# Kernel tuning notes

Hardware: AMD Instinct MI355X
Metric: run time of the kernel (lower is better)

Reference implementation:

```python
import jax, jax.numpy as jnp
import numpy as np
from jax import lax

D = 30   # embedding_dim (hardcoded in repo)
Q = 30   # question length
N = 4000 # number of sentences in doc
S = 100  # tokens per sentence
K = 5    # k_for_maxpool
SLOPE = 0.1  # LeakyReLU negative slope


def setup_inputs() -> dict:
    key = jax.random.key(0)
    ks = jax.random.split(key, 20)
    rn = lambda k, sh: jax.random.normal(k, sh, dtype=jnp.float32)
    ru = lambda k, sh: jax.random.uniform(k, sh, dtype=jnp.float32)
    return {
        "doc_sents_embeds": rn(ks[0], (N, S, D)),
        "sents_gaf": ru(ks[1], (N, 3)),
        "question_embeds": rn(ks[2], (Q, D)),
        "q_idfs": ru(ks[3], (Q, 1)),
        "doc_gaf": ru(ks[4], (4,)),
        "conv1_w": rn(ks[5], (D, D, 3)) * 0.1,
        "conv1_b": rn(ks[6], (D,)) * 0.1,
        "conv2_w": rn(ks[7], (D, D, 3)) * 0.1,
        "conv2_b": rn(ks[8], (D,)) * 0.1,
        "qw_W": rn(ks[9], (1, D + 1)) * 0.1,
        "qw_b": rn(ks[10], (1,)) * 0.1,
        "lq1_W": rn(ks[11], (8, 6)) * 0.1,
        "lq1_b": rn(ks[12], (8,)) * 0.1,
        "lq2_W": rn(ks[13], (1, 8)) * 0.1,
        "lq2_b": rn(ks[14], (1,)) * 0.1,
        "so_W": rn(ks[15], (1, 4)) * 0.1,
        "so_b": rn(ks[16], (1,)) * 0.1,
        "fl_W": rn(ks[17], (1, 5)) * 0.1,
        "fl_b": rn(ks[18], (1,)) * 0.1,
    }


def _leaky(x):
    return jnp.where(x >= 0, x, SLOPE * x)


def _conv_block(x, w, b):
    # x: [B, L, D]. torch Conv1d(D, D, 3, padding=2) then slice [1:L+1]
    # is exactly a 'same' conv with padding 1 on each side; then residual add.
    y = lax.conv_general_dilated(x.transpose(0, 2, 1), w, (1,), [(1, 1)],
                                 dimension_numbers=("NCH", "OIH", "NCH"))
    y = _leaky(y + b[None, :, None])
    return y.transpose(0, 2, 1) + x


def _cos_sim(A, B):
    # A: [Q, D], B: [N, S, D] -> [N, Q, S] (num/den as in torch my_cosine_sim)
    num = jnp.einsum("qd,nsd->nqs", A, B)
    den = jnp.linalg.norm(A, axis=-1)[None, :, None] * jnp.linalg.norm(B, axis=-1)[:, None, :]
    return num / den


def _pool(sim):
    # sort-based k-max pooling -> [max, avg_of_top_k]; sim: [N, Q, S] -> [N, Q, 2]
    vals = lax.top_k(sim, K)[0]  # descending
    return jnp.stack([vals[..., 0], vals.mean(-1)], axis=-1)


def reference(doc_sents_embeds, sents_gaf, question_embeds, q_idfs, doc_gaf,
              conv1_w, conv1_b, conv2_w, conv2_b, qw_W, qw_b,
              lq1_W, lq1_b, lq2_W, lq2_b, so_W, so_b, fl_W, fl_b):
    # question context (two residual trigram convs)
    q_conv = _conv_block(question_embeds[None], conv1_w, conv1_b)
    q_conv = _conv_block(q_conv, conv2_w, conv2_b)[0]          # [Q, D]
    # question term weights
    qw_in = jnp.concatenate([q_conv, q_idfs], axis=-1)          # [Q, D+1]
    q_weights = jax.nn.softmax((qw_in @ qw_W.T + qw_b)[:, 0])   # [Q]
    # sentence context convs (batched over all sentences)
    conv_res = _conv_block(doc_sents_embeds, conv1_w, conv1_b)
    conv_res = _conv_block(conv_res, conv2_w, conv2_b)          # [N, S, D]
    # similarity matrices
    sim_insens = _cos_sim(question_embeds, doc_sents_embeds)    # [N, Q, S]
    sim_oh = (sim_insens > 1.0 - 1e-3).astype(sim_insens.dtype)
    sim_sens = _cos_sim(q_conv, conv_res)
    # k-max pooling and per-q tiny MLP attention
    feats = jnp.concatenate([_pool(sim_oh), _pool(sim_insens), _pool(sim_sens)], axis=-1)  # [N, Q, 6]
    lo = _leaky(feats @ lq1_W.T + lq1_b) @ lq2_W.T + lq2_b      # [N, Q, 1]
    lo = lo[..., 0] * q_weights[None, :]
    sent_emit = lo.sum(-1) / Q                                  # [N]
    # per-sentence output layer
    sent_feats = jnp.concatenate([sents_gaf, sent_emit[:, None]], axis=-1)  # [N, 4]
    sent_scores = jax.nn.sigmoid((sent_feats @ so_W.T + so_b)[:, 0])        # [N]
    # doc-level score
    doc_rep = jnp.concatenate([jnp.max(sent_scores)[None], doc_gaf])        # [5]
    final = doc_rep @ fl_W.T + fl_b                                          # [1]
    return final, sent_scores
```

## Files before the change

kernel.cpp:

```cpp
#include <hip/hip_runtime.h>
#include <hip/hip_bf16.h>

#define SLOPE 0.1f

#define OFF_QW    1816
#define OFF_QNI   1846
#define OFF_QNS   1876
#define OFF_QNN   1906
#define OFF_B1    4606
#define OFF_B2    7336
#define OFF_LQ1W  7366
#define OFF_LQ1B  7414
#define OFF_LQ2W  7422
#define OFF_LQ2B  7430
#define OFF_SOW   7431
#define OFF_SOB   7435
#define OFF_FLW   7436
#define OFF_FLB   7441
#define U16_QEA   16384
#define U16_QCA   17408
#define U16_WB1   18432
#define U16_WB2   21504

typedef __attribute__((ext_vector_type(8))) __bf16 bf16x8;
typedef __attribute__((ext_vector_type(4))) float f32x4;

union Frag { uint4 u4; uint u[4]; bf16x8 v; };

__device__ __forceinline__ float bf2f(ushort h) {
    union { uint u; float f; } c; c.u = ((uint)h) << 16; return c.f;
}
__device__ __forceinline__ ushort f2bf(float f) {
    union { float f; uint u; } c; c.f = f;
    uint u = c.u;
    return (ushort)((u + 0x7FFFu + ((u >> 16) & 1u)) >> 16);
}
__device__ __forceinline__ float ldx(const void* p, long i, int bf) {
    if (bf) return bf2f(((const ushort*)p)[i]);
    return ((const float*)p)[i];
}
__device__ __forceinline__ uint pk2(float lo, float hi) {
    uint r;
    asm("v_cvt_pk_bf16_f32 %0, %1, %2" : "=v"(r) : "v"(lo), "v"(hi));
    return r;
}
__device__ __forceinline__ float blo(uint u) { return __uint_as_float(u << 16); }
__device__ __forceinline__ float bhi(uint u) { return __uint_as_float(u & 0xFFFF0000u); }
__device__ __forceinline__ float lk(float x) { return fmaxf(x, SLOPE * x); }

#define CE(x, y) { float _hi = fmaxf(x, y), _lo = fminf(x, y); x = _hi; y = _lo; }

__device__ __forceinline__ void sort4d(float& a, float& b, float& c, float& d) {
    CE(a, b); CE(c, d); CE(a, c); CE(b, d); CE(b, c);
}
__device__ __forceinline__ void merge44_5(const float* a, const float* b, float* t) {
    t[0] = fmaxf(a[0], b[0]);
    t[1] = fmaxf(fminf(a[0], b[0]), fmaxf(a[1], b[1]));
    t[2] = fmaxf(fmaxf(fminf(a[0], b[1]), fminf(a[1], b[0])), fmaxf(a[2], b[2]));
    t[3] = fmaxf(fmaxf(fminf(a[0], b[2]), fminf(a[1], b[1])),
                 fmaxf(fminf(a[2], b[0]), fmaxf(a[3], b[3])));
    t[4] = fmaxf(fmaxf(fminf(a[0], b[3]), fminf(a[1], b[2])),
                 fmaxf(fminf(a[2], b[1]), fminf(a[3], b[0])));
}
__device__ __forceinline__ void merge54_5(const float* a, const float* b, float* t) {
    t[0] = fmaxf(a[0], b[0]);
    t[1] = fmaxf(fminf(a[0], b[0]), fmaxf(a[1], b[1]));
    t[2] = fmaxf(fmaxf(fminf(a[0], b[1]), fminf(a[1], b[0])), fmaxf(a[2], b[2]));
    t[3] = fmaxf(fmaxf(fminf(a[0], b[2]), fminf(a[1], b[1])),
                 fmaxf(fminf(a[2], b[0]), fmaxf(a[3], b[3])));
    t[4] = fmaxf(fmaxf(fmaxf(fminf(a[0], b[3]), fminf(a[1], b[2])),
                       fmaxf(fminf(a[2], b[1]), fminf(a[3], b[0]))), a[4]);
}
__device__ __forceinline__ void merge55_5(const float* a, const float* b, float* t) {
    t[0] = fmaxf(a[0], b[0]);
    t[1] = fmaxf(fminf(a[0], b[0]), fmaxf(a[1], b[1]));
    t[2] = fmaxf(fmaxf(fminf(a[0], b[1]), fminf(a[1], b[0])), fmaxf(a[2], b[2]));
    t[3] = fmaxf(fmaxf(fminf(a[0], b[2]), fminf(a[1], b[1])),
                 fmaxf(fminf(a[2], b[0]), fmaxf(a[3], b[3])));
    t[4] = fmaxf(fmaxf(fmaxf(fminf(a[0], b[3]), fminf(a[1], b[2])),
                       fmaxf(fminf(a[2], b[1]), fminf(a[3], b[0]))),
                 fmaxf(a[4], b[4]));
}

__device__ __forceinline__ int detect_bf(const void* doc_in, int tid, int* scnt) {
    if (tid == 0) *scnt = 0;
    __syncthreads();
    const ushort* p = (const ushort*)doc_in;
    int local = 0;
    for (int i = tid; i < 4096; i += 256) {
        unsigned e = (p[i] >> 7) & 0xFFu;
        if (e != 0u && (e < 100u || e > 134u)) local++;
    }
    atomicAdd(scnt, local);
    __syncthreads();
    return (*scnt > 200) ? 0 : 1;
}

__global__ __launch_bounds__(256) void k_prep(
        const void* doc_in,
        const void* qe_in, const void* qidf_in,
        const void* w1_in, const void* b1_in,
        const void* w2_in, const void* b2_in,
        const void* qwW_in, const void* qwb_in,
        const void* lq1W_in, const void* lq1b_in,
        const void* lq2W_in, const void* lq2b_in,
        const void* soW_in, const void* sob_in,
        const void* flW_in, const void* flb_in,
        float* ws) {
    const int tid = threadIdx.x;
    const int blk = blockIdx.x;
    __shared__ float QE[900], T1[900], QC[900], W[2700], IDF[32], LG[32];
    __shared__ int scnt;

    const int bf = detect_bf(doc_in, tid, &scnt);
    ushort* wsu = (ushort*)ws;

    if (blk == 1) {
        if (tid == 0) { ((int*)ws)[0] = bf; }
        if (tid < 30) ws[OFF_B1 + tid] = ldx(b1_in, tid, bf);
        if (tid < 48) ws[OFF_LQ1W + tid] = ldx(lq1W_in, tid, bf);
        if (tid < 8)  { ws[OFF_LQ1B + tid] = ldx(lq1b_in, tid, bf);
                        ws[OFF_LQ2W + tid] = ldx(lq2W_in, tid, bf); }
        if (tid < 4)  ws[OFF_SOW + tid] = ldx(soW_in, tid, bf);
        if (tid < 5)  ws[OFF_FLW + tid] = ldx(flW_in, tid, bf);
        if (tid == 1) { ws[OFF_LQ2B] = ldx(lq2b_in, 0, bf);
                        ws[OFF_SOB]  = ldx(sob_in, 0, bf);
                        ws[OFF_FLB]  = ldx(flb_in, 0, bf); }
        for (int i = tid; i < 3072; i += 256) {
            int o = i / 96, kk = i % 96;
            float v1 = 0.f;
            if (o < 30 && kk < 90) {
                int ii = kk % 30, k = kk / 30;
                v1 = ldx(w1_in, (long)o*90 + ii*3 + k, bf);
            }
            wsu[U16_WB1 + i] = f2bf(v1);
        }
        return;
    }
    if (blk == 2) {
        if (tid < 30) ws[OFF_B2 + tid] = ldx(b2_in, tid, bf);
        for (int i = tid; i < 3072; i += 256) {
            int o = i / 96, kk = i % 96;
            float v2 = 0.f;
            if (o < 30 && kk < 90) {
                int ii = kk % 30, k = kk / 30;
                v2 = ldx(w2_in, (long)o*90 + ii*3 + k, bf);
            }
            wsu[U16_WB2 + i] = f2bf(v2);
        }
        return;
    }

    if (tid == 0) { ((int*)ws)[0] = bf; }

    for (int i = tid; i < 900; i += 256) QE[i] = ldx(qe_in, i, bf);
    if (tid < 30) IDF[tid] = ldx(qidf_in, tid, bf);
    for (int i = tid; i < 2700; i += 256) W[i] = ldx(w1_in, i, bf);
    __syncthreads();

    for (int idx = tid; idx < 900; idx += 256) {
        int s = idx / 30, o = idx % 30;
        float acc = ldx(b1_in, o, bf);
        for (int k = 0; k < 3; ++k) {
            int t = s + k - 1;
            if (t < 0 || t >= 30) continue;
            for (int i = 0; i < 30; ++i) acc += QE[t*30 + i] * W[o*90 + i*3 + k];
        }
        acc = acc >= 0.f ? acc : SLOPE * acc;
        T1[idx] = acc + QE[idx];
    }
    __syncthreads();
    for (int i = tid; i < 2700; i += 256) W[i] = ldx(w2_in, i, bf);
    __syncthreads();
    for (int idx = tid; idx < 900; idx += 256) {
        int s = idx / 30, o = idx % 30;
        float acc = ldx(b2_in, o, bf);
        for (int k = 0; k < 3; ++k) {
            int t = s + k - 1;
            if (t < 0 || t >= 30) continue;
            for (int i = 0; i < 30; ++i) acc += T1[t*30 + i] * W[o*90 + i*3 + k];
        }
        acc = acc >= 0.f ? acc : SLOPE * acc;
        QC[idx] = acc + T1[idx];
    }
    __syncthreads();

    if (tid < 30) {
        float s1 = 0.f, s2 = 0.f;
        for (int d = 0; d < 30; ++d) {
            float a = QE[tid*30 + d]; s1 += a*a;
            float b = QC[tid*30 + d]; s2 += b*b;
        }
        float n1 = sqrtf(s1);
        ws[OFF_QNN + tid] = n1;
        ws[OFF_QNI + tid] = 1.0f / n1;
        ws[OFF_QNS + tid] = 1.0f / sqrtf(s2);
        float z = ldx(qwb_in, 0, bf);
        for (int d = 0; d < 30; ++d) z += QC[tid*30 + d] * ldx(qwW_in, d, bf);
        z += IDF[tid] * ldx(qwW_in, 30, bf);
        LG[tid] = z;
    }
    __syncthreads();
    if (tid == 0) {
        float m = -1e30f;
        for (int q = 0; q < 30; ++q) m = fmaxf(m, LG[q]);
        float sum = 0.f, e[30];
        for (int q = 0; q < 30; ++q) { e[q] = expf(LG[q] - m); sum += e[q]; }
        for (int q = 0; q < 30; ++q) ws[OFF_QW + q] = e[q] / sum;
    }
    for (int i = tid; i < 1024; i += 256) {
        int q = i >> 5, d = i & 31;
        float ve = (q < 30 && d < 30) ? QE[q*30 + d] : 0.f;
        float vc = (q < 30 && d < 30) ? QC[q*30 + d] : 0.f;
        wsu[U16_QEA + i] = f2bf(ve);
        wsu[U16_QCA + i] = f2bf(vc);
    }
}

__global__ __launch_bounds__(128, 4) void k_main(const void* doc_in, const void* gaf_in,
                                                 void* out, float* ws) {
    const int n = blockIdx.x;
    const int tid = threadIdx.x;
    const int bf = ((const int*)ws)[0];
    const int lane = tid & 63;
    const int wid = tid >> 6;
    const int l15 = lane & 15;
    const int quad = lane >> 4;

    __shared__ uint XA32[1546];
    __shared__ uint XB32[1546];
    __shared__ __align__(16) float INVX[112];
    __shared__ float FE[30][6];

    ushort* XAu = (ushort*)XA32;
    const ushort* wsu = (const ushort*)ws;
    const uint4* qeA = (const uint4*)(wsu + U16_QEA);
    const uint4* qcA = (const uint4*)(wsu + U16_QCA);
    const uint4* wb1 = (const uint4*)(wsu + U16_WB1);
    const uint4* wb2 = (const uint4*)(wsu + U16_WB2);

    float ga0 = ldx(gaf_in, (long)n*3 + 0, bf);
    float ga1 = ldx(gaf_in, (long)n*3 + 1, bf);
    float ga2 = ldx(gaf_in, (long)n*3 + 2, bf);

    for (int i = tid; i < 46; i += 128) {
        int j = (i < 15) ? i : (1500 + i);
        XA32[j] = 0u; XB32[j] = 0u;
    }
    if (tid >= 100 && tid < 112) INVX[tid] = 0.f;
    if (bf) {
        const uint* g = (const uint*)((const ushort*)doc_in + (size_t)n * 3000);
        for (int i = tid; i < 1500; i += 128) XA32[15 + i] = g[i];
    } else {
        const float* p = (const float*)doc_in + (size_t)n * 3000;
        for (int i = tid; i < 3000; i += 128) XAu[30 + i] = f2bf(p[i]);
    }
    __syncthreads();

    if (tid < 100) {
        const uint* r = XA32 + (tid + 1) * 15;
        float s = 0.f;
        #pragma unroll
        for (int i = 0; i < 15; ++i) {
            uint u = r[i];
            float lo = __uint_as_float(u << 16);
            float hi = __uint_as_float(u & 0xFFFF0000u);
            s += lo * lo + hi * hi;
        }
        INVX[tid] = 1.f / sqrtf(s);
    }
    __syncthreads();

    auto sim_pool = [&](const uint4* qa, int iqOff, int fbase, bool do_oh) {
        const int q = wid * 16 + l15;
        Frag b;
        b.u4 = qa[q * 4 + quad];
        f32x4 acc[7];
        #pragma unroll
        for (int mt = 0; mt < 7; ++mt) {
            int m = mt * 16 + l15;
            Frag a;
            if (m < 100) {
                int base = (m + 1) * 15 + quad * 4;
                a.u[0] = XA32[base];     a.u[1] = XA32[base + 1];
                a.u[2] = XA32[base + 2]; a.u[3] = XA32[base + 3];
            } else { a.u[0] = a.u[1] = a.u[2] = a.u[3] = 0u; }
            f32x4 z = {0.f, 0.f, 0.f, 0.f};
            acc[mt] = __builtin_amdgcn_mfma_f32_16x16x32_bf16(a.v, b.v, z, 0, 0, 0);
        }
        const float4* INVX4 = (const float4*)INVX;
        float thr = (do_oh && q < 30) ? 0.999f * ws[OFF_QNN + q] : 1e30f;
        float iq  = (q < 30) ? ws[iqOff + q] : 0.f;
        float g[7][4];
        int cnt = 0;
        #pragma unroll
        for (int mt = 0; mt < 7; ++mt) {
            float4 ix = INVX4[mt * 4 + quad];
            float ixa[4] = {ix.x, ix.y, ix.z, ix.w};
            #pragma unroll
            for (int r = 0; r < 4; ++r) {
                float u = acc[mt][r] * ixa[r];
                if (mt == 6 && (quad * 4 + r) >= 4) u = -1e30f;
                g[mt][r] = u;
                if (do_oh) cnt += (u > thr) ? 1 : 0;
            }
        }
        #pragma unroll
        for (int mt = 0; mt < 7; ++mt) sort4d(g[mt][0], g[mt][1], g[mt][2], g[mt][3]);
        float p0[5], p1[5], p2[5], q0[5], q1[5], t[5];
        merge44_5(g[0], g[1], p0);
        merge44_5(g[2], g[3], p1);
        merge44_5(g[4], g[5], p2);
        merge55_5(p0, p1, q0);
        merge54_5(p2, g[6], q1);
        merge55_5(q0, q1, t);
        #pragma unroll
        for (int d = 16; d < 64; d <<= 1) {
            float pp[5];
            pp[0] = __shfl_xor(t[0], d); pp[1] = __shfl_xor(t[1], d);
            pp[2] = __shfl_xor(t[2], d); pp[3] = __shfl_xor(t[3], d);
            pp[4] = __shfl_xor(t[4], d);
            if (do_oh) cnt += __shfl_xor(cnt, d);
            float tn[5];
            merge55_5(t, pp, tn);
            t[0] = tn[0]; t[1] = tn[1]; t[2] = tn[2]; t[3] = tn[3]; t[4] = tn[4];
        }
        if (quad == 0 && q < 30) {
            if (do_oh) {
                FE[q][0] = cnt > 0 ? 1.f : 0.f;
                FE[q][1] = (float)(cnt > 5 ? 5 : cnt) * 0.2f;
            }
            FE[q][fbase]     = t[0] * iq;
            FE[q][fbase + 1] = (t[0] + t[1] + t[2] + t[3] + t[4]) * 0.2f * iq;
        }
    };

    auto conv_phase = [&](const uint* src32, uint* dst32, const uint4* wb, int bOff,
                          int m0, int m1, int m2, int m3, bool donorm) {
        Frag wf0[3], wf1[3];
        #pragma unroll
        for (int k = 0; k < 3; ++k) {
            wf0[k].u4 = wb[l15 * 12 + k * 4 + quad];
            wf1[k].u4 = wb[(16 + l15) * 12 + k * 4 + quad];
        }
        float b40[4], b41[4];
        #pragma unroll
        for (int r = 0; r < 4; ++r) {
            int o0 = quad * 4 + r, o1 = 16 + quad * 4 + r;
            b40[r] = ws[bOff + o0];
            b41[r] = (o1 < 30) ? ws[bOff + o1] : 0.f;
        }
        auto do_mt = [&](int mt) {
            const int s = mt * 16 + l15;
            const bool sv = (s < 100);
            Frag xf[3];
            #pragma unroll
            for (int k = 0; k < 3; ++k) {
                if (sv) {
                    int base = s * 15 + k * 16 + quad * 4;
                    xf[k].u[0] = src32[base];     xf[k].u[1] = src32[base + 1];
                    xf[k].u[2] = src32[base + 2]; xf[k].u[3] = src32[base + 3];
                } else { xf[k].u[0] = xf[k].u[1] = xf[k].u[2] = xf[k].u[3] = 0u; }
            }
            f32x4 a0 = {0.f, 0.f, 0.f, 0.f}, a1 = {0.f, 0.f, 0.f, 0.f};
            #pragma unroll
            for (int k = 0; k < 3; ++k) {
                a0 = __builtin_amdgcn_mfma_f32_16x16x32_bf16(wf0[k].v, xf[k].v, a0, 0, 0, 0);
                a1 = __builtin_amdgcn_mfma_f32_16x16x32_bf16(wf1[k].v, xf[k].v, a1, 0, 0, 0);
            }
            float ss = 0.f;
            if (sv) {
                const int db = (s + 1) * 15 + quad * 2;
                uint u0 = src32[db],     u1 = src32[db + 1];
                uint u2 = src32[db + 8], u3 = src32[db + 9];
                float v0 = lk(a0[0] + b40[0]) + blo(u0);
                float v1 = lk(a0[1] + b40[1]) + bhi(u0);
                float v2 = lk(a0[2] + b40[2]) + blo(u1);
                float v3 = lk(a0[3] + b40[3]) + bhi(u1);
                dst32[db]     = pk2(v0, v1);
                dst32[db + 1] = pk2(v2, v3);
                float w0 = lk(a1[0] + b41[0]) + blo(u2);
                float w1 = lk(a1[1] + b41[1]) + bhi(u2);
                dst32[db + 8] = pk2(w0, w1);
                ss = v0*v0 + v1*v1 + v2*v2 + v3*v3 + w0*w0 + w1*w1;
                if (quad < 3) {
                    float w2 = lk(a1[2] + b41[2]) + blo(u3);
                    float w3 = lk(a1[3] + b41[3]) + bhi(u3);
                    dst32[db + 9] = pk2(w2, w3);
                    ss += w2*w2 + w3*w3;
                }
            }
            if (donorm) {
                ss += __shfl_xor(ss, 16);
                ss += __shfl_xor(ss, 32);
                if (quad == 0 && sv) INVX[s] = 1.f / sqrtf(ss);
            }
        };
        do_mt(m0); do_mt(m1); do_mt(m2);
        if (m3 >= 0) do_mt(m3);
    };

    sim_pool(qeA, OFF_QNI, 2, true);
    if (wid == 0) conv_phase(XA32, XB32, wb1, OFF_B1, 0, 2, 4, -1, false);
    else          conv_phase(XA32, XB32, wb1, OFF_B1, 1, 3, 5,  6, false);
    __syncthreads();

    if (wid == 0) conv_phase(XB32, XA32, wb2, OFF_B2, 0, 2, 4,  6, true);
    else          conv_phase(XB32, XA32, wb2, OFF_B2, 1, 3, 5, -1, true);
    __syncthreads();

    sim_pool(qcA, OFF_QNS, 4, false);
    __syncthreads();

    if (wid == 0) {
        float val = 0.f;
        if (lane < 30) {
            float lo = ws[OFF_LQ2B];
            #pragma unroll
            for (int j = 0; j < 8; ++j) {
                float h = ws[OFF_LQ1B + j];
                #pragma unroll
                for (int f = 0; f < 6; ++f) h += FE[lane][f] * ws[OFF_LQ1W + j*6 + f];
                h = h >= 0.f ? h : SLOPE * h;
                lo += h * ws[OFF_LQ2W + j];
            }
            val = lo * ws[OFF_QW + lane];
        }
        for (int d = 32; d >= 1; d >>= 1) val += __shfl_xor(val, d);
        if (lane == 0) {
            float emit = val * (1.f / 30.f);
            float z = ws[OFF_SOB];
            z += ga0 * ws[OFF_SOW + 0];
            z += ga1 * ws[OFF_SOW + 1];
            z += ga2 * ws[OFF_SOW + 2];
            z += emit * ws[OFF_SOW + 3];
            float sc = 1.f / (1.f + expf(-z));
            if (bf) ((__hip_bfloat16*)out)[1 + n] = __float2bfloat16(sc);
            else    ((float*)out)[1 + n] = sc;
        }
    }
}

__global__ __launch_bounds__(256) void k_final(const void* docgaf_in, void* out, const float* ws) {
    const int tid = threadIdx.x;
    const int bf = ((const int*)ws)[0];
    __shared__ float red[256];
    float m = -1e30f;
    for (int i = tid; i < 4000; i += 256) {
        float v = bf ? __bfloat162float(((const __hip_bfloat16*)out)[1 + i])
                     : ((const float*)out)[1 + i];
        m = fmaxf(m, v);
    }
    red[tid] = m;
    __syncthreads();
    for (int off = 128; off > 0; off >>= 1) {
        if (tid < off) red[tid] = fmaxf(red[tid], red[tid + off]);
        __syncthreads();
    }
    if (tid == 0) {
        float f = ws[OFF_FLB] + red[0] * ws[OFF_FLW + 0];
        for (int i = 0; i < 4; ++i) f += ldx(docgaf_in, i, bf) * ws[OFF_FLW + 1 + i];
        if (bf) ((__hip_bfloat16*)out)[0] = __float2bfloat16(f);
        else    ((float*)out)[0] = f;
    }
}

extern "C" void kernel_launch(void* const* d_in, const int* in_sizes, int n_in,
                              void* d_out, int out_size, void* d_ws, size_t ws_size,
                              hipStream_t stream) {
    float* ws = (float*)d_ws;
    k_prep<<<3, 256, 0, stream>>>(d_in[0], d_in[2], d_in[3], d_in[5], d_in[6], d_in[7], d_in[8],
                                  d_in[9], d_in[10], d_in[11], d_in[12], d_in[13], d_in[14],
                                  d_in[15], d_in[16], d_in[17], d_in[18], ws);
    k_main<<<4000, 128, 0, stream>>>(d_in[0], d_in[1], d_out, ws);
    k_final<<<1, 256, 0, stream>>>(d_in[4], d_out, ws);
}
```

Measured before the change: 172.9 us.

## Process one sentence per wavefront with padded LDS layout and in-place convs

Each 64-lane wave now handles a whole sentence, with two sentences per 128-thread block and 2000 blocks. Because a wave owns its data, block barriers become lgkmcnt waits. The LDS row stride is padded from 15 to 16 words so fragments load as uint4, and the row norms are computed during the global load with shuffles. Both convolutions now update one buffer in place, with a software-pipelined prefetch of the next tile's fragments. This is meant to remove __syncthreads overhead and scalar LDS traffic, at the cost of more serial MFMA work per wave and reliance on the in-place update ordering being correct.

Result: slower. 179.1 us (+3.6%).

```diff
diff --git a/kernel.cpp b/kernel.cpp
--- a/kernel.cpp
+++ b/kernel.cpp
@@ -48,6 +48,8 @@
 __device__ __forceinline__ float bhi(uint u) { return __uint_as_float(u & 0xFFFF0000u); }
 __device__ __forceinline__ float lk(float x) { return fmaxf(x, SLOPE * x); }
 
+#define LGKM0() asm volatile("s_waitcnt lgkmcnt(0)" ::: "memory")
+
 #define CE(x, y) { float _hi = fmaxf(x, y), _lo = fminf(x, y); x = _hi; y = _lo; }
 
 __device__ __forceinline__ void sort4d(float& a, float& b, float& c, float& d) {
@@ -128,11 +130,9 @@
                         ws[OFF_FLB]  = ldx(flb_in, 0, bf); }
         for (int i = tid; i < 3072; i += 256) {
             int o = i / 96, kk = i % 96;
+            int k = kk >> 5, ii = kk & 31;
             float v1 = 0.f;
-            if (o < 30 && kk < 90) {
-                int ii = kk % 30, k = kk / 30;
-                v1 = ldx(w1_in, (long)o*90 + ii*3 + k, bf);
-            }
+            if (o < 30 && ii < 30) v1 = ldx(w1_in, (long)o*90 + ii*3 + k, bf);
             wsu[U16_WB1 + i] = f2bf(v1);
         }
         return;
@@ -141,11 +141,9 @@
         if (tid < 30) ws[OFF_B2 + tid] = ldx(b2_in, tid, bf);
         for (int i = tid; i < 3072; i += 256) {
             int o = i / 96, kk = i % 96;
+            int k = kk >> 5, ii = kk & 31;
             float v2 = 0.f;
-            if (o < 30 && kk < 90) {
-                int ii = kk % 30, k = kk / 30;
-                v2 = ldx(w2_in, (long)o*90 + ii*3 + k, bf);
-            }
+            if (o < 30 && ii < 30) v2 = ldx(w2_in, (long)o*90 + ii*3 + k, bf);
             wsu[U16_WB2 + i] = f2bf(v2);
         }
         return;
@@ -217,22 +215,25 @@
     }
 }
 
-__global__ __launch_bounds__(128, 4) void k_main(const void* doc_in, const void* gaf_in,
+__global__ __launch_bounds__(128, 5) void k_main(const void* doc_in, const void* gaf_in,
                                                  void* out, float* ws) {
-    const int n = blockIdx.x;
     const int tid = threadIdx.x;
-    const int bf = ((const int*)ws)[0];
     const int lane = tid & 63;
     const int wid = tid >> 6;
+    const int n = blockIdx.x * 2 + wid;
+    const int bf = ((const int*)ws)[0];
     const int l15 = lane & 15;
     const int quad = lane >> 4;
 
-    __shared__ uint XA32[1546];
-    __shared__ uint XB32[1546];
-    __shared__ __align__(16) float INVX[112];
-    __shared__ float FE[30][6];
-
-    ushort* XAu = (ushort*)XA32;
+    __shared__ __align__(16) uint Xs[2][1648];
+    __shared__ __align__(16) float INVXs[2][112];
+    __shared__ float FEs[2][30][6];
+
+    uint* X = Xs[wid];
+    uint4* X4 = (uint4*)X;
+    float* INVX = INVXs[wid];
+    float (*FE)[6] = FEs[wid];
+
     const ushort* wsu = (const ushort*)ws;
     const uint4* qeA = (const uint4*)(wsu + U16_QEA);
     const uint4* qcA = (const uint4*)(wsu + U16_QCA);
@@ -243,36 +244,42 @@
     float ga1 = ldx(gaf_in, (long)n*3 + 1, bf);
     float ga2 = ldx(gaf_in, (long)n*3 + 2, bf);
 
-    for (int i = tid; i < 46; i += 128) {
-        int j = (i < 15) ? i : (1500 + i);
-        XA32[j] = 0u; XB32[j] = 0u;
-    }
-    if (tid >= 100 && tid < 112) INVX[tid] = 0.f;
-    if (bf) {
-        const uint* g = (const uint*)((const ushort*)doc_in + (size_t)n * 3000);
-        for (int i = tid; i < 1500; i += 128) XA32[15 + i] = g[i];
-    } else {
-        const float* p = (const float*)doc_in + (size_t)n * 3000;
-        for (int i = tid; i < 3000; i += 128) XAu[30 + i] = f2bf(p[i]);
-    }
-    __syncthreads();
-
-    if (tid < 100) {
-        const uint* r = XA32 + (tid + 1) * 15;
-        float s = 0.f;
-        #pragma unroll
-        for (int i = 0; i < 15; ++i) {
-            uint u = r[i];
-            float lo = __uint_as_float(u << 16);
-            float hi = __uint_as_float(u & 0xFFFF0000u);
-            s += lo * lo + hi * hi;
-        }
-        INVX[tid] = 1.f / sqrtf(s);
-    }
-    __syncthreads();
-
-    auto sim_pool = [&](const uint4* qa, int iqOff, int fbase, bool do_oh) {
-        const int q = wid * 16 + l15;
+    {
+        uint4 z4 = make_uint4(0u, 0u, 0u, 0u);
+        if (lane < 12) X4[(lane < 4) ? lane : (400 + lane)] = z4;
+        if (lane >= 12 && lane < 24) INVX[100 + (lane - 12)] = 0.f;
+    }
+    for (int g = lane; g < 400; g += 64) {
+        int r = g >> 2, t = g & 3;
+        uint4 w;
+        float s2;
+        if (bf) {
+            const uint* gp = (const uint*)doc_in + (size_t)n * 1500 + r * 15 + t * 4;
+            uint a = gp[0], b = gp[1], c = gp[2];
+            uint d = (t < 3) ? gp[3] : 0u;
+            w = make_uint4(a, b, c, d);
+            float x0 = blo(a), x1 = bhi(a), x2 = blo(b), x3 = bhi(b);
+            float x4 = blo(c), x5 = bhi(c), x6 = blo(d), x7 = bhi(d);
+            s2 = x0*x0 + x1*x1 + x2*x2 + x3*x3 + x4*x4 + x5*x5 + x6*x6 + x7*x7;
+        } else {
+            const float* p = (const float*)doc_in + (size_t)n * 3000 + r * 30 + t * 8;
+            float2 f0 = ((const float2*)p)[0];
+            float2 f1 = ((const float2*)p)[1];
+            float2 f2 = ((const float2*)p)[2];
+            float2 f3 = (t < 3) ? ((const float2*)p)[3] : make_float2(0.f, 0.f);
+            w = make_uint4(pk2(f0.x, f0.y), pk2(f1.x, f1.y), pk2(f2.x, f2.y), pk2(f3.x, f3.y));
+            s2 = f0.x*f0.x + f0.y*f0.y + f1.x*f1.x + f1.y*f1.y
+               + f2.x*f2.x + f2.y*f2.y + f3.x*f3.x + f3.y*f3.y;
+        }
+        X4[(r + 1) * 4 + t] = w;
+        s2 += __shfl_xor(s2, 1);
+        s2 += __shfl_xor(s2, 2);
+        if (t == 0) INVX[r] = 1.f / sqrtf(s2);
+    }
+    LGKM0();
+
+    auto sim_pool = [&](const uint4* qa, int iqOff, int fbase, bool do_oh, int qbase) {
+        const int q = qbase + l15;
         Frag b;
         b.u4 = qa[q * 4 + quad];
         f32x4 acc[7];
@@ -280,11 +287,8 @@
         for (int mt = 0; mt < 7; ++mt) {
             int m = mt * 16 + l15;
             Frag a;
-            if (m < 100) {
-                int base = (m + 1) * 15 + quad * 4;
-                a.u[0] = XA32[base];     a.u[1] = XA32[base + 1];
-                a.u[2] = XA32[base + 2]; a.u[3] = XA32[base + 3];
-            } else { a.u[0] = a.u[1] = a.u[2] = a.u[3] = 0u; }
+            if (m < 100) a.u4 = X4[(m + 1) * 4 + quad];
+            else         a.u4 = make_uint4(0u, 0u, 0u, 0u);
             f32x4 z = {0.f, 0.f, 0.f, 0.f};
             acc[mt] = __builtin_amdgcn_mfma_f32_16x16x32_bf16(a.v, b.v, z, 0, 0, 0);
         }
@@ -335,8 +339,7 @@
         }
     };
 
-    auto conv_phase = [&](const uint* src32, uint* dst32, const uint4* wb, int bOff,
-                          int m0, int m1, int m2, int m3, bool donorm) {
+    auto conv_inplace = [&](const uint4* wb, int bOff, bool donorm) {
         Frag wf0[3], wf1[3];
         #pragma unroll
         for (int k = 0; k < 3; ++k) {
@@ -346,48 +349,60 @@
         float b40[4], b41[4];
         #pragma unroll
         for (int r = 0; r < 4; ++r) {
-            int o0 = quad * 4 + r, o1 = 16 + quad * 4 + r;
+            int o0 = quad * 4 + r, o1 = 16 + o0;
             b40[r] = ws[bOff + o0];
             b41[r] = (o1 < 30) ? ws[bOff + o1] : 0.f;
         }
-        auto do_mt = [&](int mt) {
+        auto load_xf = [&](int mt, Frag& f0, Frag& f1, Frag& f2) {
+            int s = mt * 16 + l15;
+            if (s < 100) {
+                f0.u4 = X4[s * 4 + quad];
+                f1.u4 = X4[(s + 1) * 4 + quad];
+                f2.u4 = X4[(s + 2) * 4 + quad];
+            } else {
+                f0.u4 = f1.u4 = f2.u4 = make_uint4(0u, 0u, 0u, 0u);
+            }
+        };
+        Frag xf0, xf1, xf2;
+        load_xf(0, xf0, xf1, xf2);
+        #pragma unroll
+        for (int mt = 0; mt < 7; ++mt) {
             const int s = mt * 16 + l15;
             const bool sv = (s < 100);
-            Frag xf[3];
-            #pragma unroll
-            for (int k = 0; k < 3; ++k) {
-                if (sv) {
-                    int base = s * 15 + k * 16 + quad * 4;
-                    xf[k].u[0] = src32[base];     xf[k].u[1] = src32[base + 1];
-                    xf[k].u[2] = src32[base + 2]; xf[k].u[3] = src32[base + 3];
-                } else { xf[k].u[0] = xf[k].u[1] = xf[k].u[2] = xf[k].u[3] = 0u; }
-            }
+            const int db = (s + 1) * 16 + quad * 2;
+            uint u0 = 0u, u1 = 0u, u2 = 0u, u3 = 0u;
+            if (sv) {
+                uint2 ua = *(const uint2*)(X + db);
+                uint2 ub = *(const uint2*)(X + db + 8);
+                u0 = ua.x; u1 = ua.y; u2 = ub.x; u3 = ub.y;
+            }
+            Frag xn0, xn1, xn2;
+            if (mt < 6) load_xf(mt + 1, xn0, xn1, xn2);
             f32x4 a0 = {0.f, 0.f, 0.f, 0.f}, a1 = {0.f, 0.f, 0.f, 0.f};
-            #pragma unroll
-            for (int k = 0; k < 3; ++k) {
-                a0 = __builtin_amdgcn_mfma_f32_16x16x32_bf16(wf0[k].v, xf[k].v, a0, 0, 0, 0);
-                a1 = __builtin_amdgcn_mfma_f32_16x16x32_bf16(wf1[k].v, xf[k].v, a1, 0, 0, 0);
-            }
+            a0 = __builtin_amdgcn_mfma_f32_16x16x32_bf16(wf0[0].v, xf0.v, a0, 0, 0, 0);
+            a1 = __builtin_amdgcn_mfma_f32_16x16x32_bf16(wf1[0].v, xf0.v, a1, 0, 0, 0);
+            a0 = __builtin_amdgcn_mfma_f32_16x16x32_bf16(wf0[1].v, xf1.v, a0, 0, 0, 0);
+            a1 = __builtin_amdgcn_mfma_f32_16x16x32_bf16(wf1[1].v, xf1.v, a1, 0, 0, 0);
+            a0 = __builtin_amdgcn_mfma_f32_16x16x32_bf16(wf0[2].v, xf2.v, a0, 0, 0, 0);
+            a1 = __builtin_amdgcn_mfma_f32_16x16x32_bf16(wf1[2].v, xf2.v, a1, 0, 0, 0);
+            LGKM0();
             float ss = 0.f;
             if (sv) {
-                const int db = (s + 1) * 15 + quad * 2;
-                uint u0 = src32[db],     u1 = src32[db + 1];
-                uint u2 = src32[db + 8], u3 = src32[db + 9];
                 float v0 = lk(a0[0] + b40[0]) + blo(u0);
                 float v1 = lk(a0[1] + b40[1]) + bhi(u0);
                 float v2 = lk(a0[2] + b40[2]) + blo(u1);
                 float v3 = lk(a0[3] + b40[3]) + bhi(u1);
-                dst32[db]     = pk2(v0, v1);
-                dst32[db + 1] = pk2(v2, v3);
+                *(uint2*)(X + db) = make_uint2(pk2(v0, v1), pk2(v2, v3));
                 float w0 = lk(a1[0] + b41[0]) + blo(u2);
                 float w1 = lk(a1[1] + b41[1]) + bhi(u2);
-                dst32[db + 8] = pk2(w0, w1);
                 ss = v0*v0 + v1*v1 + v2*v2 + v3*v3 + w0*w0 + w1*w1;
                 if (quad < 3) {
                     float w2 = lk(a1[2] + b41[2]) + blo(u3);
                     float w3 = lk(a1[3] + b41[3]) + bhi(u3);
-                    dst32[db + 9] = pk2(w2, w3);
+                    *(uint2*)(X + db + 8) = make_uint2(pk2(w0, w1), pk2(w2, w3));
                     ss += w2*w2 + w3*w3;
+                } else {
+                    X[db + 8] = pk2(w0, w1);
                 }
             }
             if (donorm) {
@@ -395,49 +410,47 @@
                 ss += __shfl_xor(ss, 32);
                 if (quad == 0 && sv) INVX[s] = 1.f / sqrtf(ss);
             }
-        };
-        do_mt(m0); do_mt(m1); do_mt(m2);
-        if (m3 >= 0) do_mt(m3);
+            xf0 = xn0; xf1 = xn1; xf2 = xn2;
+        }
     };
 
-    sim_pool(qeA, OFF_QNI, 2, true);
-    if (wid == 0) conv_phase(XA32, XB32, wb1, OFF_B1, 0, 2, 4, -1, false);
-    else          conv_phase(XA32, XB32, wb1, OFF_B1, 1, 3, 5,  6, false);
-    __syncthreads();
-
-    if (wid == 0) conv_phase(XB32, XA32, wb2, OFF_B2, 0, 2, 4,  6, true);
-    else          conv_phase(XB32, XA32, wb2, OFF_B2, 1, 3, 5, -1, true);
-    __syncthreads();
-
-    sim_pool(qcA, OFF_QNS, 4, false);
-    __syncthreads();
-
-    if (wid == 0) {
-        float val = 0.f;
-        if (lane < 30) {
-            float lo = ws[OFF_LQ2B];
+    sim_pool(qeA, OFF_QNI, 2, true, 0);
+    sim_pool(qeA, OFF_QNI, 2, true, 16);
+
+    conv_inplace(wb1, OFF_B1, false);
+    LGKM0();
+    conv_inplace(wb2, OFF_B2, true);
+    LGKM0();
+
+    sim_pool(qcA, OFF_QNS, 4, false, 0);
+    sim_pool(qcA, OFF_QNS, 4, false, 16);
+    LGKM0();
+
+    float val = 0.f;
+    if (lane < 30) {
+        float lo = ws[OFF_LQ2B];
+        #pragma unroll
+        for (int j = 0; j < 8; ++j) {
+            float h = ws[OFF_LQ1B + j];
             #pragma unroll
-            for (int j = 0; j < 8; ++j) {
-                float h = ws[OFF_LQ1B + j];
-                #pragma unroll
-                for (int f = 0; f < 6; ++f) h += FE[lane][f] * ws[OFF_LQ1W + j*6 + f];
-                h = h >= 0.f ? h : SLOPE * h;
-                lo += h * ws[OFF_LQ2W + j];
-            }
-            val = lo * ws[OFF_QW + lane];
-        }
-        for (int d = 32; d >= 1; d >>= 1) val += __shfl_xor(val, d);
-        if (lane == 0) {
-            float emit = val * (1.f / 30.f);
-            float z = ws[OFF_SOB];
-            z += ga0 * ws[OFF_SOW + 0];
-            z += ga1 * ws[OFF_SOW + 1];
-            z += ga2 * ws[OFF_SOW + 2];
-            z += emit * ws[OFF_SOW + 3];
-            float sc = 1.f / (1.f + expf(-z));
-            if (bf) ((__hip_bfloat16*)out)[1 + n] = __float2bfloat16(sc);
-            else    ((float*)out)[1 + n] = sc;
-        }
+            for (int f = 0; f < 6; ++f) h += FE[lane][f] * ws[OFF_LQ1W + j*6 + f];
+            h = lk(h);
+            lo += h * ws[OFF_LQ2W + j];
+        }
+        val = lo * ws[OFF_QW + lane];
+    }
+    #pragma unroll
+    for (int d = 32; d >= 1; d >>= 1) val += __shfl_xor(val, d);
+    if (lane == 0) {
+        float emit = val * (1.f / 30.f);
+        float z = ws[OFF_SOB];
+        z += ga0 * ws[OFF_SOW + 0];
+        z += ga1 * ws[OFF_SOW + 1];
+        z += ga2 * ws[OFF_SOW + 2];
+        z += emit * ws[OFF_SOW + 3];
+        float sc = 1.f / (1.f + expf(-z));
+        if (bf) ((__hip_bfloat16*)out)[1 + n] = __float2bfloat16(sc);
+        else    ((float*)out)[1 + n] = sc;
     }
 }
 
@@ -472,6 +485,6 @@
     k_prep<<<3, 256, 0, stream>>>(d_in[0], d_in[2], d_in[3], d_in[5], d_in[6], d_in[7], d_in[8],
                                   d_in[9], d_in[10], d_in[11], d_in[12], d_in[13], d_in[14],
                                   d_in[15], d_in[16], d_in[17], d_in[18], ws);
-    k_main<<<4000, 128, 0, stream>>>(d_in[0], d_in[1], d_out, ws);
+    k_main<<<2000, 128, 0, stream>>>(d_in[0], d_in[1], d_out, ws);
     k_final<<<1, 256, 0, stream>>>(d_in[4], d_out, ws);
 }
```

## Run conv blocks in place on a single LDS buffer to raise occupancy

Applied to the files above, without the earlier changes.

Replaces the two ping-pong LDS buffers with one buffer updated in place. The split between the two waves is now contiguous row ranges, and the rows at the boundary are mirrored into spare slots so neither wave reads a row the other has already overwritten. The weight layout is changed to a 32-aligned k stride so each row fragment can be reused across the three conv taps with a rolling prefetch, and launch bounds rise to 5 blocks per CU. The doc load is also vectorised to uint4/float4. The in-place scheme with mirrored boundary rows is fragile, and the higher occupancy target may cause register spills.

After: 174.9 us. Within noise of the previous version (+1.1%).

```diff
diff --git a/kernel.cpp b/kernel.cpp
--- a/kernel.cpp
+++ b/kernel.cpp
@@ -22,6 +22,8 @@
 #define U16_WB1   18432
 #define U16_WB2   21504
 
+#define XDW 1620
+
 typedef __attribute__((ext_vector_type(8))) __bf16 bf16x8;
 typedef __attribute__((ext_vector_type(4))) float f32x4;
 
@@ -128,11 +130,9 @@
                         ws[OFF_FLB]  = ldx(flb_in, 0, bf); }
         for (int i = tid; i < 3072; i += 256) {
             int o = i / 96, kk = i % 96;
+            int k = kk >> 5, ii = kk & 31;
             float v1 = 0.f;
-            if (o < 30 && kk < 90) {
-                int ii = kk % 30, k = kk / 30;
-                v1 = ldx(w1_in, (long)o*90 + ii*3 + k, bf);
-            }
+            if (o < 30 && ii < 30) v1 = ldx(w1_in, (long)o*90 + ii*3 + k, bf);
             wsu[U16_WB1 + i] = f2bf(v1);
         }
         return;
@@ -141,11 +141,9 @@
         if (tid < 30) ws[OFF_B2 + tid] = ldx(b2_in, tid, bf);
         for (int i = tid; i < 3072; i += 256) {
             int o = i / 96, kk = i % 96;
+            int k = kk >> 5, ii = kk & 31;
             float v2 = 0.f;
-            if (o < 30 && kk < 90) {
-                int ii = kk % 30, k = kk / 30;
-                v2 = ldx(w2_in, (long)o*90 + ii*3 + k, bf);
-            }
+            if (o < 30 && ii < 30) v2 = ldx(w2_in, (long)o*90 + ii*3 + k, bf);
             wsu[U16_WB2 + i] = f2bf(v2);
         }
         return;
@@ -217,7 +215,7 @@
     }
 }
 
-__global__ __launch_bounds__(128, 4) void k_main(const void* doc_in, const void* gaf_in,
+__global__ __launch_bounds__(128, 5) void k_main(const void* doc_in, const void* gaf_in,
                                                  void* out, float* ws) {
     const int n = blockIdx.x;
     const int tid = threadIdx.x;
@@ -227,12 +225,10 @@
     const int l15 = lane & 15;
     const int quad = lane >> 4;
 
-    __shared__ uint XA32[1546];
-    __shared__ uint XB32[1546];
+    __shared__ __align__(16) uint X[XDW];
     __shared__ __align__(16) float INVX[112];
     __shared__ float FE[30][6];
 
-    ushort* XAu = (ushort*)XA32;
     const ushort* wsu = (const ushort*)ws;
     const uint4* qeA = (const uint4*)(wsu + U16_QEA);
     const uint4* qcA = (const uint4*)(wsu + U16_QCA);
@@ -243,22 +239,31 @@
     float ga1 = ldx(gaf_in, (long)n*3 + 1, bf);
     float ga2 = ldx(gaf_in, (long)n*3 + 2, bf);
 
-    for (int i = tid; i < 46; i += 128) {
-        int j = (i < 15) ? i : (1500 + i);
-        XA32[j] = 0u; XB32[j] = 0u;
+    if (tid < 60) {
+        int j = (tid < 15) ? tid : ((tid < 45) ? (1500 + tid) : (1560 + tid));
+        X[j] = 0u;
     }
     if (tid >= 100 && tid < 112) INVX[tid] = 0.f;
     if (bf) {
-        const uint* g = (const uint*)((const ushort*)doc_in + (size_t)n * 3000);
-        for (int i = tid; i < 1500; i += 128) XA32[15 + i] = g[i];
+        const uint4* g = (const uint4*)((const ushort*)doc_in + (size_t)n * 3000);
+        for (int j = tid; j < 375; j += 128) {
+            uint4 v = g[j];
+            int d = 15 + 4 * j;
+            X[d] = v.x; X[d + 1] = v.y; X[d + 2] = v.z; X[d + 3] = v.w;
+        }
     } else {
-        const float* p = (const float*)doc_in + (size_t)n * 3000;
-        for (int i = tid; i < 3000; i += 128) XAu[30 + i] = f2bf(p[i]);
+        const float4* p4 = (const float4*)((const float*)doc_in + (size_t)n * 3000);
+        for (int j = tid; j < 750; j += 128) {
+            float4 f = p4[j];
+            int d = 15 + 2 * j;
+            X[d]     = pk2(f.x, f.y);
+            X[d + 1] = pk2(f.z, f.w);
+        }
     }
     __syncthreads();
 
     if (tid < 100) {
-        const uint* r = XA32 + (tid + 1) * 15;
+        const uint* r = X + (tid + 1) * 15;
         float s = 0.f;
         #pragma unroll
         for (int i = 0; i < 15; ++i) {
@@ -268,6 +273,13 @@
             s += lo * lo + hi * hi;
         }
         INVX[tid] = 1.f / sqrtf(s);
+    } else if (tid < 115) {
+        X[103*15 + (tid - 100)] = X[48*15 + (tid - 100)];
+    } else if (tid < 128 + 2) {  }
+    if (tid >= 100 && tid < 115) {  }
+    if (tid < 15 || true) {  }
+    if (tid >= 113 && tid < 128) {
+        X[104*15 + (tid - 113)] = X[49*15 + (tid - 113)];
     }
     __syncthreads();
 
@@ -282,8 +294,8 @@
             Frag a;
             if (m < 100) {
                 int base = (m + 1) * 15 + quad * 4;
-                a.u[0] = XA32[base];     a.u[1] = XA32[base + 1];
-                a.u[2] = XA32[base + 2]; a.u[3] = XA32[base + 3];
+                a.u[0] = X[base];     a.u[1] = X[base + 1];
+                a.u[2] = X[base + 2]; a.u[3] = X[base + 3];
             } else { a.u[0] = a.u[1] = a.u[2] = a.u[3] = 0u; }
             f32x4 z = {0.f, 0.f, 0.f, 0.f};
             acc[mt] = __builtin_amdgcn_mfma_f32_16x16x32_bf16(a.v, b.v, z, 0, 0, 0);
@@ -335,8 +347,10 @@
         }
     };
 
-    auto conv_phase = [&](const uint* src32, uint* dst32, const uint4* wb, int bOff,
-                          int m0, int m1, int m2, int m3, bool donorm) {
+    auto conv_inplace = [&](const uint4* wb, int bOff, int mirIn48, int mirIn49,
+                            bool dupOut, bool donorm) {
+        const int mtb = wid ? 3 : 0;
+        const int mte = wid ? 6 : 2;
         Frag wf0[3], wf1[3];
         #pragma unroll
         for (int k = 0; k < 3; ++k) {
@@ -346,48 +360,81 @@
         float b40[4], b41[4];
         #pragma unroll
         for (int r = 0; r < 4; ++r) {
-            int o0 = quad * 4 + r, o1 = 16 + quad * 4 + r;
+            int o0 = quad * 4 + r, o1 = 16 + o0;
             b40[r] = ws[bOff + o0];
             b41[r] = (o1 < 30) ? ws[bOff + o1] : 0.f;
         }
-        auto do_mt = [&](int mt) {
+        auto load_row = [&](int row) {
+            int rr = row;
+            if (wid == 1 && row == 48) rr = mirIn48;
+            if (wid == 0 && row == 49) rr = mirIn49;
+            Frag f;
+            int base = rr * 15 + quad * 4;
+            f.u[0] = X[base];     f.u[1] = X[base + 1];
+            f.u[2] = X[base + 2]; f.u[3] = X[base + 3];
+            return f;
+        };
+        Frag zf; zf.u[0] = zf.u[1] = zf.u[2] = zf.u[3] = 0u;
+        Frag f0n = (mtb * 16 + l15 < 100) ? load_row(mtb * 16 + l15) : zf;
+        for (int mt = mtb; mt <= mte; ++mt) {
             const int s = mt * 16 + l15;
             const bool sv = (s < 100);
-            Frag xf[3];
-            #pragma unroll
-            for (int k = 0; k < 3; ++k) {
-                if (sv) {
-                    int base = s * 15 + k * 16 + quad * 4;
-                    xf[k].u[0] = src32[base];     xf[k].u[1] = src32[base + 1];
-                    xf[k].u[2] = src32[base + 2]; xf[k].u[3] = src32[base + 3];
-                } else { xf[k].u[0] = xf[k].u[1] = xf[k].u[2] = xf[k].u[3] = 0u; }
+            Frag f0 = f0n, f1 = zf, f2 = zf;
+            if (sv) { f1 = load_row(s + 1); f2 = load_row(s + 2); }
+            if (mt < mte) {
+                int s2 = (mt + 1) * 16 + l15;
+                f0n = (s2 < 100) ? load_row(s2) : zf;
+            }
+            const int db = (s + 1) * 15 + quad * 2;
+            uint u0 = 0u, u1 = 0u, u2 = 0u, u3 = 0u;
+            if (sv) {
+                uint2 ua = *(const uint2*)(X + db);
+                uint2 ub = *(const uint2*)(X + db + 8);
+                u0 = ua.x; u1 = ua.y; u2 = ub.x; u3 = ub.y;
             }
             f32x4 a0 = {0.f, 0.f, 0.f, 0.f}, a1 = {0.f, 0.f, 0.f, 0.f};
-            #pragma unroll
-            for (int k = 0; k < 3; ++k) {
-                a0 = __builtin_amdgcn_mfma_f32_16x16x32_bf16(wf0[k].v, xf[k].v, a0, 0, 0, 0);
-                a1 = __builtin_amdgcn_mfma_f32_16x16x32_bf16(wf1[k].v, xf[k].v, a1, 0, 0, 0);
-            }
+            a0 = __builtin_amdgcn_mfma_f32_16x16x32_bf16(wf0[0].v, f0.v, a0, 0, 0, 0);
+            a1 = __builtin_amdgcn_mfma_f32_16x16x32_bf16(wf1[0].v, f0.v, a1, 0, 0, 0);
+            a0 = __builtin_amdgcn_mfma_f32_16x16x32_bf16(wf0[1].v, f1.v, a0, 0, 0, 0);
+            a1 = __builtin_amdgcn_mfma_f32_16x16x32_bf16(wf1[1].v, f1.v, a1, 0, 0, 0);
+            a0 = __builtin_amdgcn_mfma_f32_16x16x32_bf16(wf0[2].v, f2.v, a0, 0, 0, 0);
+            a1 = __builtin_amdgcn_mfma_f32_16x16x32_bf16(wf1[2].v, f2.v, a1, 0, 0, 0);
+            __builtin_amdgcn_sched_barrier(0);
             float ss = 0.f;
             if (sv) {
-                const int db = (s + 1) * 15 + quad * 2;
-                uint u0 = src32[db],     u1 = src32[db + 1];
-                uint u2 = src32[db + 8], u3 = src32[db + 9];
                 float v0 = lk(a0[0] + b40[0]) + blo(u0);
                 float v1 = lk(a0[1] + b40[1]) + bhi(u0);
                 float v2 = lk(a0[2] + b40[2]) + blo(u1);
                 float v3 = lk(a0[3] + b40[3]) + bhi(u1);
-                dst32[db]     = pk2(v0, v1);
-                dst32[db + 1] = pk2(v2, v3);
+                uint s01 = pk2(v0, v1), s23 = pk2(v2, v3);
+                *(uint2*)(X + db) = make_uint2(s01, s23);
                 float w0 = lk(a1[0] + b41[0]) + blo(u2);
                 float w1 = lk(a1[1] + b41[1]) + bhi(u2);
-                dst32[db + 8] = pk2(w0, w1);
+                uint s45 = pk2(w0, w1);
                 ss = v0*v0 + v1*v1 + v2*v2 + v3*v3 + w0*w0 + w1*w1;
+                uint s67 = 0u;
                 if (quad < 3) {
                     float w2 = lk(a1[2] + b41[2]) + blo(u3);
                     float w3 = lk(a1[3] + b41[3]) + bhi(u3);
-                    dst32[db + 9] = pk2(w2, w3);
+                    s67 = pk2(w2, w3);
+                    *(uint2*)(X + db + 8) = make_uint2(s45, s67);
                     ss += w2*w2 + w3*w3;
+                } else {
+                    X[db + 8] = s45;
+                }
+                if (dupOut) {
+                    if (wid == 0 && mt == 2 && l15 == 15) {
+                        int mdb = 105*15 + quad*2;
+                        *(uint2*)(X + mdb) = make_uint2(s01, s23);
+                        if (quad < 3) *(uint2*)(X + mdb + 8) = make_uint2(s45, s67);
+                        else          X[mdb + 8] = s45;
+                    }
+                    if (wid == 1 && mt == 3 && l15 == 0) {
+                        int mdb = 106*15 + quad*2;
+                        *(uint2*)(X + mdb) = make_uint2(s01, s23);
+                        if (quad < 3) *(uint2*)(X + mdb + 8) = make_uint2(s45, s67);
+                        else          X[mdb + 8] = s45;
+                    }
                 }
             }
             if (donorm) {
@@ -395,18 +442,16 @@
                 ss += __shfl_xor(ss, 32);
                 if (quad == 0 && sv) INVX[s] = 1.f / sqrtf(ss);
             }
-        };
-        do_mt(m0); do_mt(m1); do_mt(m2);
-        if (m3 >= 0) do_mt(m3);
+        }
     };
 
     sim_pool(qeA, OFF_QNI, 2, true);
-    if (wid == 0) conv_phase(XA32, XB32, wb1, OFF_B1, 0, 2, 4, -1, false);
-    else          conv_phase(XA32, XB32, wb1, OFF_B1, 1, 3, 5,  6, false);
-    __syncthreads();
-
-    if (wid == 0) conv_phase(XB32, XA32, wb2, OFF_B2, 0, 2, 4,  6, true);
-    else          conv_phase(XB32, XA32, wb2, OFF_B2, 1, 3, 5, -1, true);
+    __syncthreads();
+
+    conv_inplace(wb1, OFF_B1, 103, 104, true, false);
+    __syncthreads();
+
+    conv_inplace(wb2, OFF_B2, 105, 106, false, true);
     __syncthreads();
 
     sim_pool(qcA, OFF_QNS, 4, false);
@@ -421,11 +466,12 @@
                 float h = ws[OFF_LQ1B + j];
                 #pragma unroll
                 for (int f = 0; f < 6; ++f) h += FE[lane][f] * ws[OFF_LQ1W + j*6 + f];
-                h = h >= 0.f ? h : SLOPE * h;
+                h = lk(h);
                 lo += h * ws[OFF_LQ2W + j];
             }
             val = lo * ws[OFF_QW + lane];
         }
+        #pragma unroll
         for (int d = 32; d >= 1; d >>= 1) val += __shfl_xor(val, d);
         if (lane == 0) {
             float emit = val * (1.f / 30.f);
```
